# Performance work log

Measured on AMD Instinct MI355X. Metric: run time of the kernel, lower is better.

Reference implementation:

```python
import jax, jax.numpy as jnp
import numpy as np

E, S, F = 64, 128, 640
H, C, L = 256, 32, 20
EPS = 1e-5

def _bn(x, g, b, m, v):
    # eval-mode BatchNorm1d over the channel (last) axis
    return (x - m) * (g / jnp.sqrt(v + EPS)) + b

def _prelu(x, a):
    return jnp.where(x >= 0, x, a * x)

def setup_inputs() -> dict:
    key = jax.random.key(0)
    ks = jax.random.split(key, 16)
    w = 0.05  # weight scale to keep gates unsaturated
    inp = {
        'h_w_action': jax.random.normal(ks[0], (E, S, F), jnp.float32),
        'W_lin': jax.random.normal(ks[1], (H, F), jnp.float32) * w,
        'b_lin': jnp.zeros((H,), jnp.float32),
        'g1': jnp.ones((H,), jnp.float32), 'beta1': jnp.zeros((H,), jnp.float32),
        'm1': jax.random.normal(ks[2], (H,), jnp.float32) * 0.1,
        'v1': jax.random.uniform(ks[3], (H,), jnp.float32, 0.5, 1.5),
        'a1': jnp.full((1,), 0.25, jnp.float32),
        'W_ih': jax.random.normal(ks[4], (3 * H, H), jnp.float32) * w,
        'W_hh': jax.random.normal(ks[5], (3 * H, H), jnp.float32) * w,
        'b_ih': jnp.zeros((3 * H,), jnp.float32),
        'b_hh': jnp.zeros((3 * H,), jnp.float32),
        'g2': jnp.ones((H,), jnp.float32), 'beta2': jnp.zeros((H,), jnp.float32),
        'm2': jax.random.normal(ks[6], (H,), jnp.float32) * 0.1,
        'v2': jax.random.uniform(ks[7], (H,), jnp.float32, 0.5, 1.5),
        'a2': jnp.full((1,), 0.25, jnp.float32),
        'Wc': jax.random.normal(ks[8], (H, H), jnp.float32) * w,
        'bc': jnp.zeros((H,), jnp.float32),
        'g3': jnp.ones((H,), jnp.float32), 'beta3': jnp.zeros((H,), jnp.float32),
        'm3': jax.random.normal(ks[9], (H,), jnp.float32) * 0.1,
        'v3': jax.random.uniform(ks[10], (H,), jnp.float32, 0.5, 1.5),
        'a3': jnp.full((1,), 0.25, jnp.float32),
        'W_mu': jax.random.normal(ks[11], (C, H), jnp.float32) * w,
        'b_mu': jnp.zeros((C,), jnp.float32),
    }
    return inp

def reference(h_w_action, W_lin, b_lin, g1, beta1, m1, v1, a1,
              W_ih, W_hh, b_ih, b_hh, g2, beta2, m2, v2, a2,
              Wc, bc, g3, beta3, m3, v3, a3, W_mu, b_mu):
    e, s, f = h_w_action.shape
    B = e * s
    x = h_w_action.reshape(B, f) @ W_lin.T + b_lin          # [B,H] comm_lin
    x = _prelu(_bn(x, g1, beta1, m1, v1), a1)               # batchnorm block (eval, dropout=id)

    # GRU fed the same 1-step input L times, carrying hidden state
    gi_r, gi_z, gi_n = jnp.split(x @ W_ih.T + b_ih, 3, axis=-1)

    def step(h, _):
        gh_r, gh_z, gh_n = jnp.split(h @ W_hh.T + b_hh, 3, axis=-1)
        r = jax.nn.sigmoid(gi_r + gh_r)
        z = jax.nn.sigmoid(gi_z + gh_z)
        n = jnp.tanh(gi_n + r * gh_n)
        h = (1.0 - z) * n + z * h
        return h, h

    h0 = jnp.zeros_like(x)
    _, hs = jax.lax.scan(step, h0, None, length=L)          # [L,B,H]
    ch = jnp.transpose(hs, (1, 0, 2))                       # [B,L,H]

    y = _prelu(_bn(ch, g2, beta2, m2, v2), a2)              # BN+PReLU (dropout=id)
    y = jnp.einsum('blh,oh->blo', y, Wc) + bc               # k=1 Conv1d == pointwise linear
    y = _prelu(_bn(y, g3, beta3, m3, v3), a3)               # BN+PReLU

    pred = y @ W_mu.T + b_mu                                # comm_out_mu head
    return pred.reshape(e, s, L, -1)
```

## Files before the change

kernel.cpp:

```cpp
#include <hip/hip_runtime.h>
#include <hip/hip_bf16.h>


typedef __attribute__((ext_vector_type(8))) short bf16x8;
typedef __attribute__((ext_vector_type(4))) float f32x4;

#define MFMA16(a, b, c) __builtin_amdgcn_mfma_f32_16x16x32_bf16((a), (b), (c), 0, 0, 0)

__device__ __forceinline__ void bar_nodrain() {
    asm volatile("s_waitcnt lgkmcnt(0)\n\ts_barrier" ::: "memory");
}

constexpr int F   = 640;
constexpr int H   = 256;
constexpr int LSTEPS = 20;
constexpr int CO  = 32;
constexpr int LDP = 264;
constexpr int BM  = 16;

constexpr size_t WHH_E  = 0;
constexpr size_t WIH_E  = 196608;
constexpr size_t WC_E   = 393216;
constexpr size_t WMU_E  = 458752;
constexpr size_t WLIN_E = 466944;
constexpr size_t PK_ELEMS = 630784;

__device__ __align__(16) unsigned short g_wpk[PK_ELEMS];
__device__ int g_flag;

__device__ __forceinline__ float bf2f(__hip_bfloat16 x) { return __bfloat162float(x); }
__device__ __forceinline__ float bfu(unsigned short s) {
    __hip_bfloat16 h = *reinterpret_cast<__hip_bfloat16*>(&s);
    return __bfloat162float(h);
}
__device__ __forceinline__ unsigned short f2bs(float f) {
    __hip_bfloat16 h = __float2bfloat16(f);
    return *reinterpret_cast<unsigned short*>(&h);
}
__device__ __forceinline__ bf16x8 lds8(const unsigned short* p) {
    return *reinterpret_cast<const bf16x8*>(p);
}
__device__ __forceinline__ bf16x8 pk8(size_t eoff) {
    return *reinterpret_cast<const bf16x8*>(g_wpk + eoff);
}
__device__ __forceinline__ float sigm(float x) {
    return 1.0f / (1.0f + __expf(-x));
}
__device__ __forceinline__ unsigned pack2(float lo, float hi) {
    return (unsigned)f2bs(lo) | ((unsigned)f2bs(hi) << 16);
}

template<bool F32>
__device__ __forceinline__ bf16x8 g8(const void* base, size_t off) {
    if constexpr (!F32) {
        return *reinterpret_cast<const bf16x8*>((const __hip_bfloat16*)base + off);
    } else {
        const float* f = (const float*)base + off;
        float4 lo = *reinterpret_cast<const float4*>(f);
        float4 hi = *reinterpret_cast<const float4*>(f + 4);
        bf16x8 r;
        r[0] = (short)f2bs(lo.x); r[1] = (short)f2bs(lo.y);
        r[2] = (short)f2bs(lo.z); r[3] = (short)f2bs(lo.w);
        r[4] = (short)f2bs(hi.x); r[5] = (short)f2bs(hi.y);
        r[6] = (short)f2bs(hi.z); r[7] = (short)f2bs(hi.w);
        return r;
    }
}

template<bool F32>
__device__ __forceinline__ float ld1(const void* base, int i) {
    if constexpr (!F32) return bf2f(((const __hip_bfloat16*)base)[i]);
    else                return ((const float*)base)[i];
}

__global__ void detect_dtype(const void* v1) {
    const unsigned short* u = (const unsigned short*)v1;
    int f32 = 0;
    for (int i = 0; i < 8; ++i) {
        unsigned short s = u[i];
        __hip_bfloat16 h = *reinterpret_cast<__hip_bfloat16*>(&s);
        float v = __bfloat162float(h);
        if (!(v >= 0.25f && v <= 2.0f)) f32 = 1;
    }
    g_flag = f32;
}

__device__ __forceinline__ unsigned short cvt1(const void* p, size_t i, bool f32) {
    if (f32) return f2bs(((const float*)p)[i]);
    return ((const unsigned short*)p)[i];
}

__global__ void prepack(const void* Wlin, const void* Wih, const void* Whh,
                        const void* Wc, const void* Wmu) {
    const bool f32 = (g_flag != 0);
    const int gid = blockIdx.x * 256 + threadIdx.x;
    const void* src;
    size_t dbase;
    int row, col0, ncols;
    if (gid < 24576) {
        int idx = gid;
        int lane = idx & 63, j = (idx >> 6) & 1, kk = (idx >> 7) & 7;
        int t2 = idx >> 10, g = t2 % 3, w = t2 / 3;
        row = g * 256 + w * 32 + j * 16 + (lane & 15);
        col0 = kk * 32 + (lane >> 4) * 8;
        ncols = 256; src = Whh; dbase = WHH_E + (size_t)idx * 8;
    } else if (gid < 49152) {
        int idx = gid - 24576;
        int lane = idx & 63, j = (idx >> 6) & 1, kk = (idx >> 7) & 7;
        int t2 = idx >> 10, g = t2 % 3, w = t2 / 3;
        row = g * 256 + w * 32 + j * 16 + (lane & 15);
        col0 = kk * 32 + (lane >> 4) * 8;
        ncols = 256; src = Wih; dbase = WIH_E + (size_t)idx * 8;
    } else if (gid < 57344) {
        int idx = gid - 49152;
        int lane = idx & 63, j = (idx >> 6) & 1, kk = (idx >> 7) & 7, w = idx >> 10;
        row = w * 32 + j * 16 + (lane & 15);
        col0 = kk * 32 + (lane >> 4) * 8;
        ncols = 256; src = Wc; dbase = WC_E + (size_t)idx * 8;
    } else if (gid < 58368) {
        int idx = gid - 57344;
        int lane = idx & 63, kk = (idx >> 6) & 7, w = idx >> 9;
        row = w * 16 + (lane & 15);
        col0 = kk * 32 + (lane >> 4) * 8;
        ncols = 256; src = Wmu; dbase = WMU_E + (size_t)idx * 8;
    } else if (gid < 78848) {
        int idx = gid - 58368;
        int lane = idx & 63, j = (idx >> 6) & 1;
        int t1 = idx >> 7, kk = t1 % 20, w = t1 / 20;
        row = w * 32 + j * 16 + (lane & 15);
        col0 = kk * 32 + (lane >> 4) * 8;
        ncols = 640; src = Wlin; dbase = WLIN_E + (size_t)idx * 8;
    } else {
        return;
    }
    const size_t s0 = (size_t)row * ncols + col0;
    #pragma unroll
    for (int i = 0; i < 8; ++i) g_wpk[dbase + i] = cvt1(src, s0 + i, f32);
}

template<bool F32>
__device__ __forceinline__ void fast_pipe(
    const void* hw, const void* blin,
    const void* g1, const void* be1, const void* m1, const void* v1, const void* a1,
    const void* bih, const void* bhh,
    const void* g2, const void* be2, const void* m2, const void* v2, const void* a2,
    const void* bc,
    const void* g3, const void* be3, const void* m3, const void* v3, const void* a3,
    const void* bmu,
    void* out,
    unsigned short (*hb)[BM * LDP],
    unsigned short (*yb)[BM * LDP],
    unsigned short (*zb)[BM * LDP])
{
    const int tid  = threadIdx.x;
    const int cg   = tid >> 6;
    const int lane = tid & 63;
    const int m16  = lane & 15;
    const int q    = lane >> 4;
    const int row0 = blockIdx.x * BM;
    const int c0 = cg * 32 + m16;
    const int c1 = c0 + 16;
    const int cc2[2] = { c0, c1 };
    const size_t lane8 = (size_t)lane * 8;

    float s2v[2], t2v[2], s3v[2], t3f[2], bhhn[2];
    #pragma unroll
    for (int j = 0; j < 2; ++j) {
        const int cc = cc2[j];
        float s;
        s = ld1<F32>(g2, cc) * rsqrtf(ld1<F32>(v2, cc) + 1e-5f);
        s2v[j] = s; t2v[j] = ld1<F32>(be2, cc) - ld1<F32>(m2, cc) * s;
        s = ld1<F32>(g3, cc) * rsqrtf(ld1<F32>(v3, cc) + 1e-5f);
        s3v[j] = s;
        t3f[j] = (ld1<F32>(bc, cc) - ld1<F32>(m3, cc)) * s + ld1<F32>(be3, cc);
        bhhn[j] = ld1<F32>(bhh, 2 * H + cc);
    }
    const float a2v = ld1<F32>(a2, 0), a3v = ld1<F32>(a3, 0);

    {
        f32x4 xacc[2] = {};
        #pragma unroll 5
        for (int kk = 0; kk < F / 32; ++kk) {
            bf16x8 fa0 = g8<F32>(hw, (size_t)(row0 + m16) * F + kk * 32 + q * 8);
            bf16x8 b0 = pk8(WLIN_E + (size_t)((cg * 20 + kk) * 2 + 0) * 512 + lane8);
            bf16x8 b1 = pk8(WLIN_E + (size_t)((cg * 20 + kk) * 2 + 1) * 512 + lane8);
            xacc[0] = MFMA16(fa0, b0, xacc[0]);
            xacc[1] = MFMA16(fa0, b1, xacc[1]);
        }
        #pragma unroll
        for (int j = 0; j < 2; ++j) {
            const int cc = cc2[j];
            float s = ld1<F32>(g1, cc) * rsqrtf(ld1<F32>(v1, cc) + 1e-5f);
            float t = ld1<F32>(be1, cc) - ld1<F32>(m1, cc) * s;
            float bl = ld1<F32>(blin, cc);
            float av = ld1<F32>(a1, 0);
            #pragma unroll
            for (int r = 0; r < 4; ++r) {
                float vv = (xacc[j][r] + bl) * s + t;
                vv = (vv >= 0.0f) ? vv : av * vv;
                yb[0][(q * 4 + r) * LDP + cc] = f2bs(vv);
            }
        }
    }
    __syncthreads();

    unsigned girz[2][4];
    f32x4 gin[2];
    {
        f32x4 ga[3][2] = {};
        const unsigned short* xa0 = yb[0] + m16 * LDP + q * 8;
        #pragma unroll
        for (int kk = 0; kk < 8; ++kk) {
            bf16x8 fa0 = lds8(xa0 + kk * 32);
            #pragma unroll
            for (int g = 0; g < 3; ++g) {
                bf16x8 b0 = pk8(WIH_E + (size_t)(((cg * 3 + g) * 8 + kk) * 2 + 0) * 512 + lane8);
                bf16x8 b1 = pk8(WIH_E + (size_t)(((cg * 3 + g) * 8 + kk) * 2 + 1) * 512 + lane8);
                ga[g][0] = MFMA16(fa0, b0, ga[g][0]);
                ga[g][1] = MFMA16(fa0, b1, ga[g][1]);
            }
        }
        #pragma unroll
        for (int j = 0; j < 2; ++j) {
            const float br = ld1<F32>(bih, 0 * H + cc2[j]) + ld1<F32>(bhh, 0 * H + cc2[j]);
            const float bz = ld1<F32>(bih, 1 * H + cc2[j]) + ld1<F32>(bhh, 1 * H + cc2[j]);
            const float bn = ld1<F32>(bih, 2 * H + cc2[j]);
            #pragma unroll
            for (int r = 0; r < 4; ++r)
                girz[j][r] = pack2(ga[0][j][r] + br, ga[1][j][r] + bz);
            #pragma unroll
            for (int r = 0; r < 4; ++r) gin[j][r] = ga[2][j][r] + bn;
        }
    }
    __syncthreads();

    unsigned short hs[2][4];
    #pragma unroll
    for (int j = 0; j < 2; ++j)
        #pragma unroll
        for (int r = 0; r < 4; ++r) hs[j][r] = 0;

    const int nto = cg & 1;
    const float bmuv = (cg < 2) ? ld1<F32>(bmu, nto * 16 + m16) : 0.0f;

    auto do_wc = [&](int prv) {
        f32x4 w2[2] = {};
        const unsigned short* ya0 = yb[prv] + m16 * LDP + q * 8;
        #pragma unroll
        for (int kk = 0; kk < 8; ++kk) {
            bf16x8 fa0 = lds8(ya0 + kk * 32);
            bf16x8 b0 = pk8(WC_E + (size_t)((cg * 8 + kk) * 2 + 0) * 512 + lane8);
            bf16x8 b1 = pk8(WC_E + (size_t)((cg * 8 + kk) * 2 + 1) * 512 + lane8);
            w2[0] = MFMA16(fa0, b0, w2[0]);
            w2[1] = MFMA16(fa0, b1, w2[1]);
        }
        #pragma unroll
        for (int j = 0; j < 2; ++j)
            #pragma unroll
            for (int r = 0; r < 4; ++r) {
                float z0 = w2[j][r] * s3v[j] + t3f[j];
                z0 = (z0 >= 0.0f) ? z0 : a3v * z0;
                zb[prv][(q * 4 + r) * LDP + cc2[j]] = f2bs(z0);
            }
    };

    auto do_wmu = [&](int cur, int ts) {
        if (cg < 2) {
            const unsigned short* za = zb[cur] + m16 * LDP + q * 8;
            f32x4 o = {};
            #pragma unroll
            for (int kk = 0; kk < 8; ++kk) {
                bf16x8 a = lds8(za + kk * 32);
                bf16x8 b = pk8(WMU_E + (size_t)(nto * 8 + kk) * 512 + lane8);
                o = MFMA16(a, b, o);
            }
            #pragma unroll
            for (int r = 0; r < 4; ++r) {
                float vv = o[r] + bmuv;
                const size_t oi = (size_t)(row0 + q * 4 + r) * (LSTEPS * CO)
                                + ts * CO + nto * 16 + m16;
                if constexpr (F32) ((float*)out)[oi] = vv;
                else               ((__hip_bfloat16*)out)[oi] = __float2bfloat16(vv);
            }
        }
    };

    auto do_rec = [&](int cur, int prv, bool hasGh) {
        f32x4 gh[3][2] = {};
        if (hasGh) {
            const unsigned short* ha0 = hb[prv] + m16 * LDP + q * 8;
            bf16x8 pre[2][6];
            #pragma unroll
            for (int kk = 0; kk < 2; ++kk)
                #pragma unroll
                for (int g = 0; g < 3; ++g)
                    #pragma unroll
                    for (int j = 0; j < 2; ++j)
                        pre[kk][g * 2 + j] =
                            pk8(WHH_E + (size_t)(((cg * 3 + g) * 8 + kk) * 2 + j) * 512 + lane8);
            #pragma unroll
            for (int kk = 0; kk < 8; ++kk) {
                bf16x8 b00 = pre[kk & 1][0];
                bf16x8 b01 = pre[kk & 1][1];
                bf16x8 b10 = pre[kk & 1][2];
                bf16x8 b11 = pre[kk & 1][3];
                bf16x8 b20 = pre[kk & 1][4];
                bf16x8 b21 = pre[kk & 1][5];
                if (kk < 6) {
                    #pragma unroll
                    for (int g = 0; g < 3; ++g)
                        #pragma unroll
                        for (int j = 0; j < 2; ++j)
                            pre[kk & 1][g * 2 + j] =
                                pk8(WHH_E + (size_t)(((cg * 3 + g) * 8 + (kk + 2)) * 2 + j) * 512 + lane8);
                }
                bf16x8 fa0 = lds8(ha0 + kk * 32);
                gh[0][0] = MFMA16(fa0, b00, gh[0][0]);
                gh[0][1] = MFMA16(fa0, b01, gh[0][1]);
                gh[1][0] = MFMA16(fa0, b10, gh[1][0]);
                gh[1][1] = MFMA16(fa0, b11, gh[1][1]);
                gh[2][0] = MFMA16(fa0, b20, gh[2][0]);
                gh[2][1] = MFMA16(fa0, b21, gh[2][1]);
            }
        }
        #pragma unroll
        for (int j = 0; j < 2; ++j)
            #pragma unroll
            for (int r = 0; r < 4; ++r) {
                unsigned u = girz[j][r];
                float rr = sigm(bfu((unsigned short)(u & 0xffffu)) + gh[0][j][r]);
                float zz = sigm(bfu((unsigned short)(u >> 16)) + gh[1][j][r]);
                float nin = gin[j][r] + rr * (gh[2][j][r] + bhhn[j]);
                float nn = 2.0f * sigm(2.0f * nin) - 1.0f;
                float hh = (1.0f - zz) * nn + zz * bfu(hs[j][r]);
                unsigned short hv = f2bs(hh);
                hs[j][r] = hv;
                const int idx = (q * 4 + r) * LDP + cc2[j];
                hb[cur][idx] = hv;
                float y = bfu(hv) * s2v[j] + t2v[j];
                y = (y >= 0.0f) ? y : a2v * y;
                yb[cur][idx] = f2bs(y);
            }
    };

    do_rec(0, 1, false);
    bar_nodrain();
    do_wc(0);
    do_rec(1, 0, true);
    bar_nodrain();
    #pragma unroll 1
    for (int t = 2; t < LSTEPS; ++t) {
        const int cur = t & 1, prv = cur ^ 1;
        do_wc(prv);
        do_wmu(cur, t - 2);
        do_rec(cur, prv, true);
        bar_nodrain();
    }
    {
        const int cur = LSTEPS & 1, prv = cur ^ 1;
        do_wc(prv);
        do_wmu(cur, LSTEPS - 2);
        bar_nodrain();
    }
    {
        const int cur = (LSTEPS + 1) & 1;
        do_wmu(cur, LSTEPS - 1);
    }
}

__global__ __launch_bounds__(512, 2) void comm_fast(
    const void* hw, const void* blin,
    const void* g1, const void* be1, const void* m1, const void* v1, const void* a1,
    const void* bih, const void* bhh,
    const void* g2, const void* be2, const void* m2, const void* v2, const void* a2,
    const void* bc,
    const void* g3, const void* be3, const void* m3, const void* v3, const void* a3,
    const void* bmu,
    void* out)
{
    __shared__ __align__(16) unsigned short hb[2][BM * LDP];
    __shared__ __align__(16) unsigned short yb[2][BM * LDP];
    __shared__ __align__(16) unsigned short zb[2][BM * LDP];
    if (g_flag) {
        fast_pipe<true >(hw, blin, g1, be1, m1, v1, a1, bih, bhh,
                         g2, be2, m2, v2, a2, bc, g3, be3, m3, v3, a3, bmu,
                         out, hb, yb, zb);
    } else {
        fast_pipe<false>(hw, blin, g1, be1, m1, v1, a1, bih, bhh,
                         g2, be2, m2, v2, a2, bc, g3, be3, m3, v3, a3, bmu,
                         out, hb, yb, zb);
    }
}

extern "C" void kernel_launch(void* const* d_in, const int* in_sizes, int n_in,
                              void* d_out, int out_size, void* d_ws, size_t ws_size,
                              hipStream_t stream) {
    (void)in_sizes; (void)n_in; (void)out_size; (void)d_ws; (void)ws_size;
    detect_dtype<<<dim3(1), dim3(1), 0, stream>>>(d_in[6]);
    prepack<<<dim3(308), dim3(256), 0, stream>>>(
        d_in[1], d_in[8], d_in[9], d_in[17], d_in[24]);
    comm_fast<<<dim3(512), dim3(512), 0, stream>>>(
        d_in[0], d_in[2],
        d_in[3], d_in[4], d_in[5], d_in[6], d_in[7],
        d_in[10], d_in[11],
        d_in[12], d_in[13], d_in[14], d_in[15], d_in[16],
        d_in[18],
        d_in[19], d_in[20], d_in[21], d_in[22], d_in[23],
        d_in[25],
        d_out);
}
```

Baseline: 441.4 us.

## Batch four GRU recurrence steps before running conv and head stages

The time loop is restructured. Before, each step ran the pointwise conv, the output head and the recurrence under a single barrier. Now four recurrence steps run back to back, each writing its BN/PReLU output into its own slot of a four-slot LDS ring. The conv and mu-head stages for those four timesteps then run as a separate pipelined phase. The aim is to keep the serial recurrence chain free of conv and head work, but it roughly doubles the number of block barriers, removes the overlap of independent work within a step, and grows LDS use per block.

```diff
diff --git a/kernel.cpp b/kernel.cpp
--- a/kernel.cpp
+++ b/kernel.cpp
@@ -149,7 +149,7 @@
     const void* bmu,
     void* out,
     unsigned short (*hb)[BM * LDP],
-    unsigned short (*yb)[BM * LDP],
+    unsigned short (*yr)[BM * LDP],
     unsigned short (*zb)[BM * LDP])
 {
     const int tid  = threadIdx.x;
@@ -198,7 +198,7 @@
             for (int r = 0; r < 4; ++r) {
                 float vv = (xacc[j][r] + bl) * s + t;
                 vv = (vv >= 0.0f) ? vv : av * vv;
-                yb[0][(q * 4 + r) * LDP + cc] = f2bs(vv);
+                yr[3][(q * 4 + r) * LDP + cc] = f2bs(vv);
             }
         }
     }
@@ -208,7 +208,7 @@
     f32x4 gin[2];
     {
         f32x4 ga[3][2] = {};
-        const unsigned short* xa0 = yb[0] + m16 * LDP + q * 8;
+        const unsigned short* xa0 = yr[3] + m16 * LDP + q * 8;
         #pragma unroll
         for (int kk = 0; kk < 8; ++kk) {
             bf16x8 fa0 = lds8(xa0 + kk * 32);
@@ -243,49 +243,7 @@
     const int nto = cg & 1;
     const float bmuv = (cg < 2) ? ld1<F32>(bmu, nto * 16 + m16) : 0.0f;
 
-    auto do_wc = [&](int prv) {
-        f32x4 w2[2] = {};
-        const unsigned short* ya0 = yb[prv] + m16 * LDP + q * 8;
-        #pragma unroll
-        for (int kk = 0; kk < 8; ++kk) {
-            bf16x8 fa0 = lds8(ya0 + kk * 32);
-            bf16x8 b0 = pk8(WC_E + (size_t)((cg * 8 + kk) * 2 + 0) * 512 + lane8);
-            bf16x8 b1 = pk8(WC_E + (size_t)((cg * 8 + kk) * 2 + 1) * 512 + lane8);
-            w2[0] = MFMA16(fa0, b0, w2[0]);
-            w2[1] = MFMA16(fa0, b1, w2[1]);
-        }
-        #pragma unroll
-        for (int j = 0; j < 2; ++j)
-            #pragma unroll
-            for (int r = 0; r < 4; ++r) {
-                float z0 = w2[j][r] * s3v[j] + t3f[j];
-                z0 = (z0 >= 0.0f) ? z0 : a3v * z0;
-                zb[prv][(q * 4 + r) * LDP + cc2[j]] = f2bs(z0);
-            }
-    };
-
-    auto do_wmu = [&](int cur, int ts) {
-        if (cg < 2) {
-            const unsigned short* za = zb[cur] + m16 * LDP + q * 8;
-            f32x4 o = {};
-            #pragma unroll
-            for (int kk = 0; kk < 8; ++kk) {
-                bf16x8 a = lds8(za + kk * 32);
-                bf16x8 b = pk8(WMU_E + (size_t)(nto * 8 + kk) * 512 + lane8);
-                o = MFMA16(a, b, o);
-            }
-            #pragma unroll
-            for (int r = 0; r < 4; ++r) {
-                float vv = o[r] + bmuv;
-                const size_t oi = (size_t)(row0 + q * 4 + r) * (LSTEPS * CO)
-                                + ts * CO + nto * 16 + m16;
-                if constexpr (F32) ((float*)out)[oi] = vv;
-                else               ((__hip_bfloat16*)out)[oi] = __float2bfloat16(vv);
-            }
-        }
-    };
-
-    auto do_rec = [&](int cur, int prv, bool hasGh) {
+    auto do_rec = [&](int cur, int prv, int yslot, bool hasGh) {
         f32x4 gh[3][2] = {};
         if (hasGh) {
             const unsigned short* ha0 = hb[prv] + m16 * LDP + q * 8;
@@ -339,32 +297,70 @@
                 hb[cur][idx] = hv;
                 float y = bfu(hv) * s2v[j] + t2v[j];
                 y = (y >= 0.0f) ? y : a2v * y;
-                yb[cur][idx] = f2bs(y);
+                yr[yslot][idx] = f2bs(y);
             }
     };
 
-    do_rec(0, 1, false);
-    bar_nodrain();
-    do_wc(0);
-    do_rec(1, 0, true);
-    bar_nodrain();
+    auto do_wc = [&](int yslot) {
+        f32x4 w2[2] = {};
+        const unsigned short* ya0 = yr[yslot] + m16 * LDP + q * 8;
+        #pragma unroll
+        for (int kk = 0; kk < 8; ++kk) {
+            bf16x8 fa0 = lds8(ya0 + kk * 32);
+            bf16x8 b0 = pk8(WC_E + (size_t)((cg * 8 + kk) * 2 + 0) * 512 + lane8);
+            bf16x8 b1 = pk8(WC_E + (size_t)((cg * 8 + kk) * 2 + 1) * 512 + lane8);
+            w2[0] = MFMA16(fa0, b0, w2[0]);
+            w2[1] = MFMA16(fa0, b1, w2[1]);
+        }
+        #pragma unroll
+        for (int j = 0; j < 2; ++j)
+            #pragma unroll
+            for (int r = 0; r < 4; ++r) {
+                float z0 = w2[j][r] * s3v[j] + t3f[j];
+                z0 = (z0 >= 0.0f) ? z0 : a3v * z0;
+                zb[yslot & 1][(q * 4 + r) * LDP + cc2[j]] = f2bs(z0);
+            }
+    };
+
+    auto do_wmu = [&](int zpar, int ts) {
+        if (cg < 2) {
+            const unsigned short* za = zb[zpar] + m16 * LDP + q * 8;
+            f32x4 o = {};
+            #pragma unroll
+            for (int kk = 0; kk < 8; ++kk) {
+                bf16x8 a = lds8(za + kk * 32);
+                bf16x8 b = pk8(WMU_E + (size_t)(nto * 8 + kk) * 512 + lane8);
+                o = MFMA16(a, b, o);
+            }
+            #pragma unroll
+            for (int r = 0; r < 4; ++r) {
+                float vv = o[r] + bmuv;
+                const size_t oi = (size_t)(row0 + q * 4 + r) * (LSTEPS * CO)
+                                + ts * CO + nto * 16 + m16;
+                if constexpr (F32) ((float*)out)[oi] = vv;
+                else               ((__hip_bfloat16*)out)[oi] = __float2bfloat16(vv);
+            }
+        }
+    };
+
     #pragma unroll 1
-    for (int t = 2; t < LSTEPS; ++t) {
-        const int cur = t & 1, prv = cur ^ 1;
-        do_wc(prv);
-        do_wmu(cur, t - 2);
-        do_rec(cur, prv, true);
+    for (int grp = 0; grp < 5; ++grp) {
+        #pragma unroll
+        for (int k = 0; k < 4; ++k) {
+            do_rec(k & 1, (k & 1) ^ 1, k, (grp + k) > 0);
+            bar_nodrain();
+        }
+        const int t0 = grp * 4;
+        do_wc(0);
         bar_nodrain();
-    }
-    {
-        const int cur = LSTEPS & 1, prv = cur ^ 1;
-        do_wc(prv);
-        do_wmu(cur, LSTEPS - 2);
+        do_wmu(0, t0 + 0); do_wc(1);
         bar_nodrain();
-    }
-    {
-        const int cur = (LSTEPS + 1) & 1;
-        do_wmu(cur, LSTEPS - 1);
+        do_wmu(1, t0 + 1); do_wc(2);
+        bar_nodrain();
+        do_wmu(0, t0 + 2); do_wc(3);
+        bar_nodrain();
+        do_wmu(1, t0 + 3);
+        bar_nodrain();
     }
 }
 
@@ -379,16 +375,16 @@
     void* out)
 {
     __shared__ __align__(16) unsigned short hb[2][BM * LDP];
-    __shared__ __align__(16) unsigned short yb[2][BM * LDP];
+    __shared__ __align__(16) unsigned short yr[4][BM * LDP];
     __shared__ __align__(16) unsigned short zb[2][BM * LDP];
     if (g_flag) {
         fast_pipe<true >(hw, blin, g1, be1, m1, v1, a1, bih, bhh,
                          g2, be2, m2, v2, a2, bc, g3, be3, m3, v3, a3, bmu,
-                         out, hb, yb, zb);
+                         out, hb, yr, zb);
     } else {
         fast_pipe<false>(hw, blin, g1, be1, m1, v1, a1, bih, bhh,
                          g2, be2, m2, v2, a2, bc, g3, be3, m3, v3, a3, bmu,
-                         out, hb, yb, zb);
+                         out, hb, yr, zb);
     }
 }
 
```

Measured after the change: 410.6 us. -7.0%, faster.
